# Performance work log

Measured on AMD Instinct MI355X. Metric: run time of the kernel, lower is better.

The kernel has to match this reference:

```python
import jax, jax.numpy as jnp
import numpy as np

HEAD_DIM = 128
INFTY_APPROX = 1e+30
ROTARY_BASE = 10000.0

B, T, M = 2, 2048, 1024
H = M // HEAD_DIM  # 8


def setup_inputs() -> dict:
    key = jax.random.key(0)
    ks = jax.random.split(key, 5)
    x = jax.random.normal(ks[0], (B, T, M), dtype=jnp.float32)
    # mu-param inits: wq zeros in the original; use small random here for a
    # non-degenerate numerical baseline, scaled like kv_init = d_model**-0.5
    scale = M ** (-0.5)
    wq = jax.random.normal(ks[1], (M, H, HEAD_DIM), dtype=jnp.float32) * scale
    wk = jax.random.normal(ks[2], (M, H, HEAD_DIM), dtype=jnp.float32) * scale
    wv = jax.random.normal(ks[3], (M, H, HEAD_DIM), dtype=jnp.float32) * scale
    wo = jax.random.normal(ks[4], (H, HEAD_DIM, M), dtype=jnp.float32) * scale
    return {"x": x, "wq": wq, "wk": wk, "wv": wv, "wo": wo}


def _rotary(x, base=ROTARY_BASE):
    # x: [..., T, W]; non-interpretable RoPE over even/odd halves of W
    length, width = x.shape[-2], x.shape[-1]
    half = width // 2
    positions = jnp.arange(length)[:, None].astype(x.dtype)          # [T,1]
    ang_freqs = jnp.power(base, -jnp.arange(half) / half)[None, :]   # [1,half]
    radians = positions * ang_freqs                                  # [T,half]
    cos = jnp.cos(radians).astype(x.dtype)
    sin = jnp.sin(radians).astype(x.dtype)
    even, odd = jnp.split(x, 2, axis=-1)
    return jnp.concatenate([even * cos - odd * sin,
                            even * sin + odd * cos], axis=-1)


def _fractional_rotary(x):
    # rotary on first half of head dim, passthrough on the rest
    rot, skip = jnp.split(x, 2, axis=-1)
    return jnp.concatenate([_rotary(rot), skip], axis=-1)


def reference(x, wq, wk, wv, wo):
    q = jnp.einsum('bim,mhd->bhid', x, wq)
    k = jnp.einsum('bim,mhd->bhid', x, wk)
    v = jnp.einsum('bim,mhd->bhid', x, wv)
    q = _fractional_rotary(q)
    k = _fractional_rotary(k)
    # mu-param attention: scale by 1/HEAD_DIM (not 1/sqrt(D))
    s = jnp.einsum('bhid,bhjd->bhij', q, k) / HEAD_DIM
    i = jnp.arange(T)[:, None]
    j = jnp.arange(T)[None, :]
    mask = (i < j).astype(s.dtype)  # strictly-upper-triangular
    s = s - jnp.asarray(INFTY_APPROX, dtype=s.dtype) * mask
    p = jax.nn.softmax(s, axis=-1)
    o = jnp.einsum('bhij,bhjd->bhid', p, v)
    r = jnp.einsum('bhid,hdm->bim', o, wo)
    return r
```

## Files before the change

### kernel.cpp

```cpp
#include <hip/hip_runtime.h>

#define T_SEQ 2048
#define MDL   1024
#define NH    8
#define HD    128
#define SPLIT 4

typedef __bf16 bf16;
typedef __bf16 bf16x8 __attribute__((ext_vector_type(8)));
typedef __bf16 bf16x4 __attribute__((ext_vector_type(4)));
typedef float  f32x4  __attribute__((ext_vector_type(4)));

#define GLB(p) ((const __attribute__((address_space(1))) void*)(p))
#define LDS(p) ((__attribute__((address_space(3))) void*)(p))

#if __has_builtin(__builtin_amdgcn_exp2f)
#define EXP2(x) __builtin_amdgcn_exp2f(x)
#else
#define EXP2(x) __expf((x) * 0.6931471805599453f)
#endif

#define QSCALE 0.011271055f


__global__ __launch_bounds__(256) void prep_kernel(
    const float* __restrict__ x,
    const float* __restrict__ wq, const float* __restrict__ wk,
    const float* __restrict__ wv, const float* __restrict__ wo,
    bf16* __restrict__ xb, bf16* __restrict__ Wt, bf16* __restrict__ Wot)
{
    __shared__ bf16 t_lds[64 * 72];
    const int tid = threadIdx.x;
    if (blockIdx.x < 2048) {
        size_t i = ((size_t)blockIdx.x * 256 + tid) * 8;
        float4 v0 = *(const float4*)(x + i);
        float4 v1 = *(const float4*)(x + i + 4);
        bf16x8 o;
        o[0]=(bf16)v0.x; o[1]=(bf16)v0.y; o[2]=(bf16)v0.z; o[3]=(bf16)v0.w;
        o[4]=(bf16)v1.x; o[5]=(bf16)v1.y; o[6]=(bf16)v1.z; o[7]=(bf16)v1.w;
        *(bf16x8*)(xb + i) = o;
        return;
    }
    const int bx = blockIdx.x - 2048;
    const int sec = bx >> 8;
    const int tile = bx & 255;
    const int k0 = (tile >> 4) * 64, n0 = (tile & 15) * 64;
    const float* src = sec == 0 ? wq : sec == 1 ? wk : sec == 2 ? wv : wo;
    bf16* dst = sec < 3 ? (Wt + (size_t)sec * MDL * MDL) : Wot;

    const int ir = tid >> 2, jc = (tid & 3) * 16;
    const float* sp = src + (size_t)(k0 + ir) * MDL + n0 + jc;
    #pragma unroll
    for (int c = 0; c < 4; ++c) {
        float4 v = *(const float4*)(sp + c * 4);
        bf16x4 o; o[0]=(bf16)v.x; o[1]=(bf16)v.y; o[2]=(bf16)v.z; o[3]=(bf16)v.w;
        *(bf16x4*)&t_lds[ir * 72 + jc + c * 4] = o;
    }
    __syncthreads();
    bf16x8 o0, o1;
    #pragma unroll
    for (int jj = 0; jj < 8; ++jj) {
        o0[jj] = t_lds[(jc + jj) * 72 + ir];
        o1[jj] = t_lds[(jc + 8 + jj) * 72 + ir];
    }
    bf16* dp = dst + (size_t)(n0 + ir) * MDL + k0 + jc;
    *(bf16x8*)dp = o0;
    *(bf16x8*)(dp + 8) = o1;
}

__global__ __launch_bounds__(256) void qkv_rope_kernel(
    const bf16* __restrict__ xb, const bf16* __restrict__ Wt,
    bf16* __restrict__ Qb, bf16* __restrict__ Kt, bf16* __restrict__ Vt)
{
    __shared__ bf16 smem[8192];
    bf16* a_lds = smem;
    bf16* b_lds = smem + 4096;

    const int tid = threadIdx.x, bx = blockIdx.x;
    const int nt = bx % 24, mt = bx / 24;
    const int n0 = nt * 128, m0 = mt * 128;
    const int section = n0 >> 10;
    const int h = (n0 & 1023) >> 7;

    const int lane = tid & 63, w = tid >> 6;
    const int quad = lane >> 4, l15 = lane & 15;
    const int wr = w >> 1, wc = w & 1;
    const int lrow = lane >> 2, lsub = lane & 3;

    const bf16* gA = xb + (size_t)m0 * MDL + lsub * 8;
    const bf16* gB = Wt + (size_t)n0 * MDL + lsub * 8;

    f32x4 acc[4][4] = {};

    for (int k0 = 0; k0 < MDL; k0 += 32) {
        #pragma unroll
        for (int i = 0; i < 2; ++i) {
            const int ch = w * 2 + i;
            const int row = ch * 16 + lrow;
            __builtin_amdgcn_global_load_lds(GLB(gA + (size_t)row * MDL + k0),
                                             LDS(&a_lds[ch * 16 * 32]), 16, 0, 0);
            __builtin_amdgcn_global_load_lds(GLB(gB + (size_t)row * MDL + k0),
                                             LDS(&b_lds[ch * 16 * 32]), 16, 0, 0);
        }
        __syncthreads();

        bf16x8 af[4], bfr[4];
        #pragma unroll
        for (int mi = 0; mi < 4; ++mi)
            af[mi] = *(const bf16x8*)&a_lds[(wr * 64 + mi * 16 + l15) * 32 + quad * 8];
        #pragma unroll
        for (int ni = 0; ni < 4; ++ni)
            bfr[ni] = *(const bf16x8*)&b_lds[(wc * 64 + ni * 16 + l15) * 32 + quad * 8];
        #pragma unroll
        for (int mi = 0; mi < 4; ++mi)
            #pragma unroll
            for (int ni = 0; ni < 4; ++ni)
                acc[mi][ni] = __builtin_amdgcn_mfma_f32_16x16x32_bf16(af[mi], bfr[ni], acc[mi][ni], 0, 0, 0);
        __syncthreads();
    }

    const int bdx = m0 >> 11;
    const int t0 = m0 & (T_SEQ - 1);
    const int bh = bdx * NH + h;

    if (section == 2) {
        #pragma unroll
        for (int c = 0; c < 2; ++c) {
            if (wc == c) {
                #pragma unroll
                for (int mi = 0; mi < 4; ++mi)
                    #pragma unroll
                    for (int r = 0; r < 4; ++r) {
                        int p = 16 * quad + 4 * r + mi;
                        int base = (wr * 8 + (p >> 3)) * 512 + (p & 7);
                        #pragma unroll
                        for (int ni = 0; ni < 4; ++ni)
                            smem[base + (ni * 16 + l15) * 8] = (bf16)acc[mi][ni][r];
                    }
            }
            __syncthreads();
            {
                const int t8 = tid >> 4;
                bf16* vp = Vt + ((size_t)(bh * 32 + (t0 >> 6) + (t8 >> 3))) * 8192
                              + (t8 & 7) * 1024 + c * 512 + (tid & 15) * 32;
                #pragma unroll
                for (int k = 0; k < 4; ++k)
                    *(bf16x8*)(vp + k * 8) = *(const bf16x8*)&smem[tid * 32 + k * 8];
            }
            __syncthreads();
        }
        return;
    }

    float fr_n[2];
    #pragma unroll
    for (int ni = 0; ni < 2; ++ni)
        fr_n[ni] = __expf(-(float)(ni * 16 + l15) * 0.28782313662425573f);

    if (section == 0) {
        #pragma unroll
        for (int mi = 0; mi < 4; ++mi) {
            #pragma unroll
            for (int r = 0; r < 4; ++r) {
                int t = t0 + wr * 64 + mi * 16 + quad * 4 + r;
                bf16* orow = Qb + ((size_t)bh * T_SEQ + t) * HD;
                if (wc == 0) {
                    #pragma unroll
                    for (int ni = 0; ni < 2; ++ni) {
                        int d = ni * 16 + l15;
                        float ang = (float)t * fr_n[ni];
                        float sn = __sinf(ang), cs = __cosf(ang);
                        float ev = acc[mi][ni][r];
                        float ov = acc[mi][ni + 2][r];
                        orow[d]      = (bf16)((ev * cs - ov * sn) * QSCALE);
                        orow[d + 32] = (bf16)((ev * sn + ov * cs) * QSCALE);
                    }
                } else {
                    #pragma unroll
                    for (int ni = 0; ni < 4; ++ni)
                        orow[64 + ni * 16 + l15] = (bf16)(acc[mi][ni][r] * QSCALE);
                }
            }
        }
    } else {
        #pragma unroll
        for (int c = 0; c < 2; ++c) {
            if (wr == c) {
                #pragma unroll
                for (int mi = 0; mi < 4; ++mi) {
                    #pragma unroll
                    for (int r = 0; r < 4; ++r) {
                        int tl = mi * 16 + quad * 4 + r;
                        int t = t0 + c * 64 + tl;
                        if (wc == 0) {
                            #pragma unroll
                            for (int ni = 0; ni < 2; ++ni) {
                                int d = ni * 16 + l15;
                                float ang = (float)t * fr_n[ni];
                                float sn = __sinf(ang), cs = __cosf(ang);
                                float ev = acc[mi][ni][r];
                                float ov = acc[mi][ni + 2][r];
                                smem[(d >> 3) * 512 + tl * 8 + (d & 7)] = (bf16)(ev * cs - ov * sn);
                                int d2 = d + 32;
                                smem[(d2 >> 3) * 512 + tl * 8 + (d2 & 7)] = (bf16)(ev * sn + ov * cs);
                            }
                        } else {
                            #pragma unroll
                            for (int ni = 0; ni < 4; ++ni) {
                                int d = 64 + ni * 16 + l15;
                                smem[(d >> 3) * 512 + tl * 8 + (d & 7)] = (bf16)acc[mi][ni][r];
                            }
                        }
                    }
                }
            }
            __syncthreads();
            {
                bf16* kp = Kt + ((size_t)(bh * 32 + (t0 >> 6) + c)) * 8192 + tid * 32;
                #pragma unroll
                for (int k = 0; k < 4; ++k)
                    *(bf16x8*)(kp + k * 8) = *(const bf16x8*)&smem[tid * 32 + k * 8];
            }
            __syncthreads();
        }
    }
}

__global__ __launch_bounds__(256) void attn_kernel(
    const bf16* __restrict__ Qb, const bf16* __restrict__ Kt,
    const bf16* __restrict__ Vt, bf16* __restrict__ PO, float* __restrict__ Pl)
{
    __shared__ bf16 k_lds[8192];
    __shared__ bf16 v_lds[8192];
    __shared__ bf16 p_lds[4][32 * 72];

    const int tid = threadIdx.x, lane = tid & 63, w = tid >> 6;
    const int quad = lane >> 4, l15 = lane & 15;
    const int bx = blockIdx.x;
    const int s0 = bx % SPLIT;
    const int ip = (bx / SPLIT) & 7;
    const int bh = bx / (SPLIT * 8);
    const int tA = 2 * ip + 2;

    const bf16* Kbh = Kt + (size_t)bh * 32 * 8192;
    const bf16* Vbh = Vt + (size_t)bh * 32 * 8192;

    bf16x8 kreg[4], vreg[4];
    bf16x8 qf[2][4];
    f32x4 Of[2][8];
    float l_r[2][4];

    auto fetch = [&](int g) {
        const int jt = (g < tA) ? g : g - tA;
        const bf16* kt = Kbh + (size_t)jt * 8192 + tid * 8;
        const bf16* vt = Vbh + (size_t)jt * 8192 + tid * 8;
        #pragma unroll
        for (int k = 0; k < 4; ++k) {
            kreg[k] = *(const bf16x8*)(kt + k * 2048);
            vreg[k] = *(const bf16x8*)(vt + k * 2048);
        }
    };

    fetch(s0);
    int pqt = -1;

    #pragma unroll 1
    for (int g = s0; g < 34; g += SPLIT) {
        const int ph = (g >= tA);
        const int qt = ph ? 15 - ip : ip;
        const int jt = ph ? g - tA : g;

        if (qt != pqt) {
            if (pqt >= 0) {
                const size_t slot = ((size_t)bh * 16 + pqt) * SPLIT + s0;
                #pragma unroll
                for (int mi = 0; mi < 2; ++mi)
                    #pragma unroll
                    for (int r = 0; r < 4; ++r) {
                        float ls = l_r[mi][r];
                        ls += __shfl_xor(ls, 1); ls += __shfl_xor(ls, 2);
                        ls += __shfl_xor(ls, 4); ls += __shfl_xor(ls, 8);
                        const int row = w * 32 + mi * 16 + quad * 4 + r;
                        if (l15 == 0) Pl[slot * 128 + row] = ls;
                        bf16* pr = PO + (slot * 128 + row) * 128;
                        #pragma unroll
                        for (int di = 0; di < 8; ++di)
                            pr[di * 16 + l15] = (bf16)Of[mi][di][r];
                    }
            }
            #pragma unroll
            for (int mi = 0; mi < 2; ++mi) {
                const bf16* qrow = Qb + ((size_t)bh * T_SEQ + qt * 128 + w * 32 + mi * 16 + l15) * HD + quad * 8;
                #pragma unroll
                for (int kk = 0; kk < 4; ++kk)
                    qf[mi][kk] = *(const bf16x8*)(qrow + kk * 32);
                #pragma unroll
                for (int di = 0; di < 8; ++di) Of[mi][di] = (f32x4){0.f, 0.f, 0.f, 0.f};
                #pragma unroll
                for (int r = 0; r < 4; ++r) l_r[mi][r] = 0.f;
            }
            pqt = qt;
        }

        __syncthreads();
        #pragma unroll
        for (int k = 0; k < 4; ++k) {
            *(bf16x8*)&k_lds[k * 2048 + tid * 8] = kreg[k];
            *(bf16x8*)&v_lds[k * 2048 + tid * 8] = vreg[k];
        }
        if (g + SPLIT < 34) fetch(g + SPLIT);
        __syncthreads();

        f32x4 sa[2][4] = {};
        #pragma unroll
        for (int kk = 0; kk < 4; ++kk) {
            bf16x8 kb[4];
            #pragma unroll
            for (int ni = 0; ni < 4; ++ni)
                kb[ni] = *(const bf16x8*)&k_lds[(kk * 4 + quad) * 512 + (ni * 16 + l15) * 8];
            #pragma unroll
            for (int ni = 0; ni < 4; ++ni)
                #pragma unroll
                for (int mi = 0; mi < 2; ++mi)
                    sa[mi][ni] = __builtin_amdgcn_mfma_f32_16x16x32_bf16(qf[mi][kk], kb[ni], sa[mi][ni], 0, 0, 0);
        }

        const bool diag = (jt >= 2 * qt);
        #pragma unroll
        for (int mi = 0; mi < 2; ++mi) {
            const int rowb = w * 32 + mi * 16 + quad * 4;
            #pragma unroll
            for (int r = 0; r < 4; ++r) {
                float ps = 0.f;
                bf16x4 pq;
                #pragma unroll
                for (int ni = 0; ni < 4; ++ni) {
                    float pv = EXP2(sa[mi][ni][r]);
                    if (diag && (jt * 64 + ni * 16 + l15) > (qt * 128 + rowb + r)) pv = 0.f;
                    ps += pv;
                    pq[ni] = (bf16)pv;
                }
                *(bf16x4*)&p_lds[w][(mi * 16 + quad * 4 + r) * 72 + l15 * 4] = pq;
                l_r[mi][r] += ps;
            }
        }

        #pragma unroll
        for (int kk = 0; kk < 2; ++kk) {
            bf16x8 pa[2];
            #pragma unroll
            for (int mi = 0; mi < 2; ++mi)
                pa[mi] = *(const bf16x8*)&p_lds[w][(mi * 16 + l15) * 72 + kk * 32 + quad * 8];
            #pragma unroll
            for (int di = 0; di < 8; ++di) {
                bf16x8 vb = *(const bf16x8*)&v_lds[(kk * 4 + quad) * 1024 + (di * 16 + l15) * 8];
                #pragma unroll
                for (int mi = 0; mi < 2; ++mi)
                    Of[mi][di] = __builtin_amdgcn_mfma_f32_16x16x32_bf16(pa[mi], vb, Of[mi][di], 0, 0, 0);
            }
        }
    }

    {
        const size_t slot = ((size_t)bh * 16 + pqt) * SPLIT + s0;
        #pragma unroll
        for (int mi = 0; mi < 2; ++mi)
            #pragma unroll
            for (int r = 0; r < 4; ++r) {
                float ls = l_r[mi][r];
                ls += __shfl_xor(ls, 1); ls += __shfl_xor(ls, 2);
                ls += __shfl_xor(ls, 4); ls += __shfl_xor(ls, 8);
                const int row = w * 32 + mi * 16 + quad * 4 + r;
                if (l15 == 0) Pl[slot * 128 + row] = ls;
                bf16* pr = PO + (slot * 128 + row) * 128;
                #pragma unroll
                for (int di = 0; di < 8; ++di)
                    pr[di * 16 + l15] = (bf16)Of[mi][di][r];
            }
    }
}

__global__ __launch_bounds__(256) void attn_combine_kernel(
    const bf16* __restrict__ PO, const float* __restrict__ Pl,
    bf16* __restrict__ Ob)
{
    const int idx = blockIdx.x * 256 + threadIdx.x;
    const int dcol = (idx & 15) * 8;
    const int rowg = idx >> 4;
    const int bh = rowg >> 11, qrow = rowg & 2047;
    const int qt = qrow >> 7, row = qrow & 127;
    const int ns = (qt == 0) ? 2 : ((qt == 1) ? 4 : SPLIT);

    float acc[8] = {};
    float l = 0.f;
    for (int s = 0; s < ns; ++s) {
        const size_t base = (((size_t)bh * 16 + qt) * SPLIT + s) * 128 + row;
        bf16x8 po = *(const bf16x8*)&PO[base * 128 + dcol];
        #pragma unroll
        for (int jj = 0; jj < 8; ++jj) acc[jj] += (float)po[jj];
        l += Pl[base];
    }
    const float inv = 1.f / l;
    const int b = bh >> 3, hh = bh & 7, t = qt * 128 + row;
    bf16x8 o;
    #pragma unroll
    for (int jj = 0; jj < 8; ++jj) o[jj] = (bf16)(acc[jj] * inv);
    *(bf16x8*)(Ob + ((size_t)(b * T_SEQ + t) * NH + hh) * HD + dcol) = o;
}

__global__ __launch_bounds__(256) void out_proj_kernel(
    const bf16* __restrict__ Ob, const bf16* __restrict__ Wot,
    float* __restrict__ out)
{
    __shared__ bf16 a_lds[128 * 32];
    __shared__ bf16 b_lds[128 * 32];

    const int tid = threadIdx.x, bx = blockIdx.x;
    const int nt = bx & 7, mt = bx >> 3;
    const int n0 = nt * 128, m0 = mt * 128;

    const int lane = tid & 63, w = tid >> 6;
    const int quad = lane >> 4, l15 = lane & 15;
    const int wr = w >> 1, wc = w & 1;
    const int lrow = lane >> 2, lsub = lane & 3;

    const bf16* gA = Ob  + (size_t)m0 * MDL + lsub * 8;
    const bf16* gB = Wot + (size_t)n0 * MDL + lsub * 8;

    f32x4 acc[4][4] = {};

    for (int k0 = 0; k0 < MDL; k0 += 32) {
        #pragma unroll
        for (int i = 0; i < 2; ++i) {
            const int ch = w * 2 + i;
            const int row = ch * 16 + lrow;
            __builtin_amdgcn_global_load_lds(GLB(gA + (size_t)row * MDL + k0),
                                             LDS(&a_lds[ch * 16 * 32]), 16, 0, 0);
            __builtin_amdgcn_global_load_lds(GLB(gB + (size_t)row * MDL + k0),
                                             LDS(&b_lds[ch * 16 * 32]), 16, 0, 0);
        }
        __syncthreads();

        bf16x8 af[4], bfr[4];
        #pragma unroll
        for (int mi = 0; mi < 4; ++mi)
            af[mi] = *(const bf16x8*)&a_lds[(wr * 64 + mi * 16 + l15) * 32 + quad * 8];
        #pragma unroll
        for (int ni = 0; ni < 4; ++ni)
            bfr[ni] = *(const bf16x8*)&b_lds[(wc * 64 + ni * 16 + l15) * 32 + quad * 8];
        #pragma unroll
        for (int mi = 0; mi < 4; ++mi)
            #pragma unroll
            for (int ni = 0; ni < 4; ++ni)
                acc[mi][ni] = __builtin_amdgcn_mfma_f32_16x16x32_bf16(af[mi], bfr[ni], acc[mi][ni], 0, 0, 0);
        __syncthreads();
    }

    #pragma unroll
    for (int mi = 0; mi < 4; ++mi)
        #pragma unroll
        for (int r = 0; r < 4; ++r) {
            int row_g = m0 + wr * 64 + mi * 16 + quad * 4 + r;
            float* crow = out + (size_t)row_g * MDL + n0;
            #pragma unroll
            for (int ni = 0; ni < 4; ++ni)
                crow[wc * 64 + ni * 16 + l15] = acc[mi][ni][r];
        }
}

extern "C" void kernel_launch(void* const* d_in, const int* in_sizes, int n_in,
                              void* d_out, int out_size, void* d_ws, size_t ws_size,
                              hipStream_t stream) {
    const float* x  = (const float*)d_in[0];
    const float* wq = (const float*)d_in[1];
    const float* wk = (const float*)d_in[2];
    const float* wv = (const float*)d_in[3];
    const float* wo = (const float*)d_in[4];
    float* out = (float*)d_out;

    const size_t NTOK = (size_t)2 * NH * T_SEQ * HD;
    bf16*  Qb  = (bf16*)d_ws;
    bf16*  Kt  = Qb + NTOK;
    bf16*  Vt  = Kt + NTOK;
    bf16*  Ob  = Vt + NTOK;
    bf16*  Wot = Ob + NTOK;
    bf16*  PO  = Wot + (size_t)MDL * MDL;
    float* Pl  = (float*)(PO + (size_t)16 * 16 * SPLIT * 128 * 128);

    bf16* xbuf = (bf16*)d_out;
    bf16* Wt   = xbuf + (size_t)4096 * MDL;

    prep_kernel<<<3072, 256, 0, stream>>>(x, wq, wk, wv, wo, xbuf, Wt, Wot);
    qkv_rope_kernel<<<768, 256, 0, stream>>>(xbuf, Wt, Qb, Kt, Vt);
    attn_kernel<<<16 * 8 * SPLIT, 256, 0, stream>>>(Qb, Kt, Vt, PO, Pl);
    attn_combine_kernel<<<2048, 256, 0, stream>>>(PO, Pl, Ob);
    out_proj_kernel<<<256, 256, 0, stream>>>(Ob, Wot, out);
}
```

Before: 195.3 us.

## Split key tiles across waves in-block and fuse split-K combine into attention

Attention blocks now own a 32-row query tile. The four waves each take every fourth 64-key tile and load K and V straight from global memory into registers, with no LDS staging and no per-tile block barriers. Partial outputs and row sums are reduced through shared memory inside the block, which removes the separate combine kernel and its global partial buffers. The cost is lower MFMA reuse per K/V load (32 query rows per tile instead of 128), more global K/V traffic, and register pressure under the two-blocks-per-SM launch bound.

```diff
diff --git a/kernel.cpp b/kernel.cpp
--- a/kernel.cpp
+++ b/kernel.cpp
@@ -4,7 +4,6 @@
 #define MDL   1024
 #define NH    8
 #define HD    128
-#define SPLIT 4
 
 typedef __bf16 bf16;
 typedef __bf16 bf16x8 __attribute__((ext_vector_type(8)));
@@ -226,143 +225,133 @@
     }
 }
 
-__global__ __launch_bounds__(256) void attn_kernel(
+__global__ __launch_bounds__(256, 2) void attn_kernel(
     const bf16* __restrict__ Qb, const bf16* __restrict__ Kt,
-    const bf16* __restrict__ Vt, bf16* __restrict__ PO, float* __restrict__ Pl)
+    const bf16* __restrict__ Vt, bf16* __restrict__ Ob)
 {
-    __shared__ bf16 k_lds[8192];
-    __shared__ bf16 v_lds[8192];
     __shared__ bf16 p_lds[4][32 * 72];
+    __shared__ bf16 slot[4][128 * 32];
+    __shared__ float lsl[4][32];
 
     const int tid = threadIdx.x, lane = tid & 63, w = tid >> 6;
     const int quad = lane >> 4, l15 = lane & 15;
     const int bx = blockIdx.x;
-    const int s0 = bx % SPLIT;
-    const int ip = (bx / SPLIT) & 7;
-    const int bh = bx / (SPLIT * 8);
-    const int tA = 2 * ip + 2;
+    const int m  = bx & 31;
+    const int bh = bx >> 5;
+    const int b = bh >> 3, h = bh & 7;
 
     const bf16* Kbh = Kt + (size_t)bh * 32 * 8192;
     const bf16* Vbh = Vt + (size_t)bh * 32 * 8192;
 
-    bf16x8 kreg[4], vreg[4];
+    bf16x8 kb[4][4];
+    bf16x8 vb[8];
     bf16x8 qf[2][4];
     f32x4 Of[2][8];
     float l_r[2][4];
 
-    auto fetch = [&](int g) {
-        const int jt = (g < tA) ? g : g - tA;
-        const bf16* kt = Kbh + (size_t)jt * 8192 + tid * 8;
-        const bf16* vt = Vbh + (size_t)jt * 8192 + tid * 8;
-        #pragma unroll
-        for (int k = 0; k < 4; ++k) {
-            kreg[k] = *(const bf16x8*)(kt + k * 2048);
-            vreg[k] = *(const bf16x8*)(vt + k * 2048);
-        }
+    const bf16* kbase = Kbh + (size_t)quad * 512 + (size_t)l15 * 8;
+    const bf16* vbase = Vbh + (size_t)quad * 1024 + (size_t)l15 * 8;
+
+    auto issue_k = [&](int j) {
+        const bf16* kt = kbase + (size_t)j * 8192;
+        #pragma unroll
+        for (int kk = 0; kk < 4; ++kk)
+            #pragma unroll
+            for (int ni = 0; ni < 4; ++ni)
+                kb[kk][ni] = *(const bf16x8*)(kt + kk * 2048 + ni * 128);
     };
-
-    fetch(s0);
-    int pqt = -1;
+    auto issue_v = [&](int j, int half) {
+        const bf16* vt = vbase + (size_t)j * 8192 + half * 4096;
+        #pragma unroll
+        for (int di = 0; di < 8; ++di)
+            vb[di] = *(const bf16x8*)(vt + di * 128);
+    };
 
     #pragma unroll 1
-    for (int g = s0; g < 34; g += SPLIT) {
-        const int ph = (g >= tA);
-        const int qt = ph ? 15 - ip : ip;
-        const int jt = ph ? g - tA : g;
-
-        if (qt != pqt) {
-            if (pqt >= 0) {
-                const size_t slot = ((size_t)bh * 16 + pqt) * SPLIT + s0;
+    for (int phase = 0; phase < 2; ++phase) {
+        const int qt = phase ? m : 63 - m;
+        const int cnt = (qt >> 1) + 1;
+        const int dj = qt >> 1;
+
+        #pragma unroll
+        for (int mi = 0; mi < 2; ++mi) {
+            const bf16* qr = Qb + ((size_t)bh * T_SEQ + qt * 32 + mi * 16 + l15) * HD + quad * 8;
+            #pragma unroll
+            for (int kk = 0; kk < 4; ++kk)
+                qf[mi][kk] = *(const bf16x8*)(qr + kk * 32);
+            #pragma unroll
+            for (int di = 0; di < 8; ++di) Of[mi][di] = (f32x4){0.f, 0.f, 0.f, 0.f};
+            #pragma unroll
+            for (int r = 0; r < 4; ++r) l_r[mi][r] = 0.f;
+        }
+
+        if (w < cnt) issue_k(w);
+
+        #pragma unroll 1
+        for (int jt = w; jt < cnt; jt += 4) {
+            f32x4 sa[2][4] = {};
+            #pragma unroll
+            for (int kk = 0; kk < 4; ++kk)
+                #pragma unroll
+                for (int ni = 0; ni < 4; ++ni)
+                    #pragma unroll
+                    for (int mi = 0; mi < 2; ++mi)
+                        sa[mi][ni] = __builtin_amdgcn_mfma_f32_16x16x32_bf16(qf[mi][kk], kb[kk][ni], sa[mi][ni], 0, 0, 0);
+
+            if (jt + 4 < cnt) issue_k(jt + 4);
+            issue_v(jt, 0);
+
+            const bool diag = (jt == dj);
+            #pragma unroll
+            for (int mi = 0; mi < 2; ++mi) {
+                #pragma unroll
+                for (int r = 0; r < 4; ++r) {
+                    const int rowg = qt * 32 + mi * 16 + quad * 4 + r;
+                    float ps = 0.f;
+                    bf16x4 pq;
+                    #pragma unroll
+                    for (int ni = 0; ni < 4; ++ni) {
+                        float pv = EXP2(sa[mi][ni][r]);
+                        if (diag && (jt * 64 + ni * 16 + l15) > rowg) pv = 0.f;
+                        ps += pv;
+                        pq[ni] = (bf16)pv;
+                    }
+                    *(bf16x4*)&p_lds[w][(mi * 16 + quad * 4 + r) * 72 + l15 * 4] = pq;
+                    l_r[mi][r] += ps;
+                }
+            }
+
+            bf16x8 pa[2];
+            #pragma unroll
+            for (int mi = 0; mi < 2; ++mi)
+                pa[mi] = *(const bf16x8*)&p_lds[w][(mi * 16 + l15) * 72 + quad * 8];
+            #pragma unroll
+            for (int di = 0; di < 8; ++di)
                 #pragma unroll
                 for (int mi = 0; mi < 2; ++mi)
-                    #pragma unroll
-                    for (int r = 0; r < 4; ++r) {
-                        float ls = l_r[mi][r];
-                        ls += __shfl_xor(ls, 1); ls += __shfl_xor(ls, 2);
-                        ls += __shfl_xor(ls, 4); ls += __shfl_xor(ls, 8);
-                        const int row = w * 32 + mi * 16 + quad * 4 + r;
-                        if (l15 == 0) Pl[slot * 128 + row] = ls;
-                        bf16* pr = PO + (slot * 128 + row) * 128;
-                        #pragma unroll
-                        for (int di = 0; di < 8; ++di)
-                            pr[di * 16 + l15] = (bf16)Of[mi][di][r];
-                    }
-            }
-            #pragma unroll
-            for (int mi = 0; mi < 2; ++mi) {
-                const bf16* qrow = Qb + ((size_t)bh * T_SEQ + qt * 128 + w * 32 + mi * 16 + l15) * HD + quad * 8;
-                #pragma unroll
-                for (int kk = 0; kk < 4; ++kk)
-                    qf[mi][kk] = *(const bf16x8*)(qrow + kk * 32);
-                #pragma unroll
-                for (int di = 0; di < 8; ++di) Of[mi][di] = (f32x4){0.f, 0.f, 0.f, 0.f};
-                #pragma unroll
-                for (int r = 0; r < 4; ++r) l_r[mi][r] = 0.f;
-            }
-            pqt = qt;
-        }
-
-        __syncthreads();
-        #pragma unroll
-        for (int k = 0; k < 4; ++k) {
-            *(bf16x8*)&k_lds[k * 2048 + tid * 8] = kreg[k];
-            *(bf16x8*)&v_lds[k * 2048 + tid * 8] = vreg[k];
-        }
-        if (g + SPLIT < 34) fetch(g + SPLIT);
-        __syncthreads();
-
-        f32x4 sa[2][4] = {};
-        #pragma unroll
-        for (int kk = 0; kk < 4; ++kk) {
-            bf16x8 kb[4];
-            #pragma unroll
-            for (int ni = 0; ni < 4; ++ni)
-                kb[ni] = *(const bf16x8*)&k_lds[(kk * 4 + quad) * 512 + (ni * 16 + l15) * 8];
-            #pragma unroll
-            for (int ni = 0; ni < 4; ++ni)
+                    Of[mi][di] = __builtin_amdgcn_mfma_f32_16x16x32_bf16(pa[mi], vb[di], Of[mi][di], 0, 0, 0);
+
+            issue_v(jt, 1);
+            #pragma unroll
+            for (int mi = 0; mi < 2; ++mi)
+                pa[mi] = *(const bf16x8*)&p_lds[w][(mi * 16 + l15) * 72 + 32 + quad * 8];
+            #pragma unroll
+            for (int di = 0; di < 8; ++di)
                 #pragma unroll
                 for (int mi = 0; mi < 2; ++mi)
-                    sa[mi][ni] = __builtin_amdgcn_mfma_f32_16x16x32_bf16(qf[mi][kk], kb[ni], sa[mi][ni], 0, 0, 0);
-        }
-
-        const bool diag = (jt >= 2 * qt);
-        #pragma unroll
-        for (int mi = 0; mi < 2; ++mi) {
-            const int rowb = w * 32 + mi * 16 + quad * 4;
-            #pragma unroll
-            for (int r = 0; r < 4; ++r) {
-                float ps = 0.f;
-                bf16x4 pq;
-                #pragma unroll
-                for (int ni = 0; ni < 4; ++ni) {
-                    float pv = EXP2(sa[mi][ni][r]);
-                    if (diag && (jt * 64 + ni * 16 + l15) > (qt * 128 + rowb + r)) pv = 0.f;
-                    ps += pv;
-                    pq[ni] = (bf16)pv;
-                }
-                *(bf16x4*)&p_lds[w][(mi * 16 + quad * 4 + r) * 72 + l15 * 4] = pq;
-                l_r[mi][r] += ps;
-            }
-        }
-
-        #pragma unroll
-        for (int kk = 0; kk < 2; ++kk) {
-            bf16x8 pa[2];
-            #pragma unroll
-            for (int mi = 0; mi < 2; ++mi)
-                pa[mi] = *(const bf16x8*)&p_lds[w][(mi * 16 + l15) * 72 + kk * 32 + quad * 8];
+                    Of[mi][di] = __builtin_amdgcn_mfma_f32_16x16x32_bf16(pa[mi], vb[di], Of[mi][di], 0, 0, 0);
+        }
+
+        __syncthreads();
+        #pragma unroll
+        for (int mi = 0; mi < 2; ++mi)
             #pragma unroll
             for (int di = 0; di < 8; ++di) {
-                bf16x8 vb = *(const bf16x8*)&v_lds[(kk * 4 + quad) * 1024 + (di * 16 + l15) * 8];
-                #pragma unroll
-                for (int mi = 0; mi < 2; ++mi)
-                    Of[mi][di] = __builtin_amdgcn_mfma_f32_16x16x32_bf16(pa[mi], vb, Of[mi][di], 0, 0, 0);
-            }
-        }
-    }
-
-    {
-        const size_t slot = ((size_t)bh * 16 + pqt) * SPLIT + s0;
+                bf16x4 t;
+                #pragma unroll
+                for (int r = 0; r < 4; ++r) t[r] = (bf16)Of[mi][di][r];
+                *(bf16x4*)&slot[w][(di * 16 + l15) * 32 + mi * 16 + quad * 4] = t;
+            }
         #pragma unroll
         for (int mi = 0; mi < 2; ++mi)
             #pragma unroll
@@ -370,42 +359,32 @@
                 float ls = l_r[mi][r];
                 ls += __shfl_xor(ls, 1); ls += __shfl_xor(ls, 2);
                 ls += __shfl_xor(ls, 4); ls += __shfl_xor(ls, 8);
-                const int row = w * 32 + mi * 16 + quad * 4 + r;
-                if (l15 == 0) Pl[slot * 128 + row] = ls;
-                bf16* pr = PO + (slot * 128 + row) * 128;
-                #pragma unroll
-                for (int di = 0; di < 8; ++di)
-                    pr[di * 16 + l15] = (bf16)Of[mi][di][r];
-            }
-    }
-}
-
-__global__ __launch_bounds__(256) void attn_combine_kernel(
-    const bf16* __restrict__ PO, const float* __restrict__ Pl,
-    bf16* __restrict__ Ob)
-{
-    const int idx = blockIdx.x * 256 + threadIdx.x;
-    const int dcol = (idx & 15) * 8;
-    const int rowg = idx >> 4;
-    const int bh = rowg >> 11, qrow = rowg & 2047;
-    const int qt = qrow >> 7, row = qrow & 127;
-    const int ns = (qt == 0) ? 2 : ((qt == 1) ? 4 : SPLIT);
-
-    float acc[8] = {};
-    float l = 0.f;
-    for (int s = 0; s < ns; ++s) {
-        const size_t base = (((size_t)bh * 16 + qt) * SPLIT + s) * 128 + row;
-        bf16x8 po = *(const bf16x8*)&PO[base * 128 + dcol];
-        #pragma unroll
-        for (int jj = 0; jj < 8; ++jj) acc[jj] += (float)po[jj];
-        l += Pl[base];
-    }
-    const float inv = 1.f / l;
-    const int b = bh >> 3, hh = bh & 7, t = qt * 128 + row;
-    bf16x8 o;
-    #pragma unroll
-    for (int jj = 0; jj < 8; ++jj) o[jj] = (bf16)(acc[jj] * inv);
-    *(bf16x8*)(Ob + ((size_t)(b * T_SEQ + t) * NH + hh) * HD + dcol) = o;
+                if (l15 == 0) lsl[w][mi * 16 + quad * 4 + r] = ls;
+            }
+        __syncthreads();
+        {
+            const int row = tid >> 3;
+            const int dc = (tid & 7) * 16;
+            float av[16] = {};
+            float l = 0.f;
+            #pragma unroll
+            for (int s = 0; s < 4; ++s) {
+                l += lsl[s][row];
+                #pragma unroll
+                for (int c = 0; c < 16; ++c)
+                    av[c] += (float)slot[s][(dc + c) * 32 + row];
+            }
+            const float inv = 1.f / l;
+            const int t = qt * 32 + row;
+            bf16* op = Ob + ((size_t)(b * T_SEQ + t) * NH + h) * HD + dc;
+            bf16x8 o0, o1;
+            #pragma unroll
+            for (int c = 0; c < 8; ++c) { o0[c] = (bf16)(av[c] * inv); o1[c] = (bf16)(av[c + 8] * inv); }
+            *(bf16x8*)op = o0;
+            *(bf16x8*)(op + 8) = o1;
+        }
+        __syncthreads();
+    }
 }
 
 __global__ __launch_bounds__(256) void out_proj_kernel(
@@ -484,15 +463,12 @@
     bf16*  Vt  = Kt + NTOK;
     bf16*  Ob  = Vt + NTOK;
     bf16*  Wot = Ob + NTOK;
-    bf16*  PO  = Wot + (size_t)MDL * MDL;
-    float* Pl  = (float*)(PO + (size_t)16 * 16 * SPLIT * 128 * 128);
 
     bf16* xbuf = (bf16*)d_out;
     bf16* Wt   = xbuf + (size_t)4096 * MDL;
 
     prep_kernel<<<3072, 256, 0, stream>>>(x, wq, wk, wv, wo, xbuf, Wt, Wot);
     qkv_rope_kernel<<<768, 256, 0, stream>>>(xbuf, Wt, Qb, Kt, Vt);
-    attn_kernel<<<16 * 8 * SPLIT, 256, 0, stream>>>(Qb, Kt, Vt, PO, Pl);
-    attn_combine_kernel<<<2048, 256, 0, stream>>>(PO, Pl, Ob);
+    attn_kernel<<<512, 256, 0, stream>>>(Qb, Kt, Vt, Ob);
     out_proj_kernel<<<256, 256, 0, stream>>>(Ob, Wot, out);
 }
```

After: 210.1 us. 7.6% more time.
